# Performance work log

Measured on AMD Instinct MI355X. Metric: run time of the kernel, lower is better.

## Reference

```python
import jax, jax.numpy as jnp
import numpy as np
import math

B, L, D, H = 4, 1024, 1024, 16
HD = D // H

def setup_inputs() -> dict:
    rng = jax.random.key(0)
    ks = jax.random.split(rng, 11)
    def lin(k):
        # orthogonal-ish init not needed for numerics; normal scaled like torch default
        return jax.random.normal(k, (D, D), dtype=jnp.float32) * 0.02
    return {
        'key':   jax.random.normal(ks[0], (B, L, D), dtype=jnp.float32),
        'value': jax.random.normal(ks[1], (B, L, D), dtype=jnp.float32),
        'query': jax.random.normal(ks[2], (B, L, D), dtype=jnp.float32),
        'Wk': lin(ks[3]), 'bk': jnp.zeros((D,), jnp.float32),
        'Wq': lin(ks[4]), 'bq': jnp.zeros((D,), jnp.float32),
        'Wv': lin(ks[5]), 'bv': jnp.zeros((D,), jnp.float32),
        'Wp': lin(ks[6]), 'bp': jnp.zeros((D,), jnp.float32),
    }

def reference(key, value, query, Wk, bk, Wq, bq, Wv, bv, Wp, bp):
    # linear projections (torch Linear: x @ W.T + b)
    k = (key   @ Wk.T + bk).reshape(B, L, H, HD).transpose(0, 2, 1, 3)  # [B,H,L,hd]
    q = (query @ Wq.T + bq).reshape(B, L, H, HD).transpose(0, 2, 1, 3)
    v = (value @ Wv.T + bv).reshape(B, L, H, HD).transpose(0, 2, 1, 3)
    att = jnp.einsum('bhqd,bhkd->bhqk', q, k) * (1.0 / math.sqrt(HD))  # [B,H,L,L]
    causal = jnp.tril(jnp.ones((L, L), dtype=bool))
    att = jnp.where(causal[None, None], att, -jnp.inf)
    att = jax.nn.softmax(att, axis=-1)
    y = jnp.einsum('bhqk,bhkd->bhqd', att, v)  # [B,H,L,hd]
    y = y.transpose(0, 2, 1, 3).reshape(B, L, D)
    return y @ Wp.T + bp
```

## Files before the change

kernel.cpp:

```cpp
#include <hip/hip_runtime.h>

typedef unsigned short u16;
typedef __attribute__((ext_vector_type(8))) short bf16x8;
typedef __attribute__((ext_vector_type(4))) float f32x4;
typedef __attribute__((ext_vector_type(4))) unsigned short u16x4;

#define MFMA16 __builtin_amdgcn_mfma_f32_16x16x32_bf16

__device__ inline u16 f2bf(float f) {
    union { float f; unsigned u; } v; v.f = f;
    unsigned r = v.u + 0x7fffu + ((v.u >> 16) & 1u);
    return (u16)(r >> 16);
}

__device__ inline void gld16(const u16* g, u16* l) {
    __builtin_amdgcn_global_load_lds(
        (const __attribute__((address_space(1))) unsigned int*)g,
        (__attribute__((address_space(3))) unsigned int*)l, 16, 0, 0);
}

struct CvtArgs { const float* src[7]; u16* dst[7]; };

__global__ __launch_bounds__(256) void cvt_kernel(CvtArgs a) {
    const int z = blockIdx.z;
    const int n = (z < 3) ? 4194304 : 1048576;
    const size_t i = ((size_t)blockIdx.x * 256 + threadIdx.x) * 8;
    if (i >= (size_t)n) return;
    const float* s = a.src[z];
    float4 v0 = *(const float4*)(s + i);
    float4 v1 = *(const float4*)(s + i + 4);
    union { u16 h[8]; bf16x8 v; } o;
    o.h[0] = f2bf(v0.x); o.h[1] = f2bf(v0.y); o.h[2] = f2bf(v0.z); o.h[3] = f2bf(v0.w);
    o.h[4] = f2bf(v1.x); o.h[5] = f2bf(v1.y); o.h[6] = f2bf(v1.z); o.h[7] = f2bf(v1.w);
    *(bf16x8*)(a.dst[z] + i) = o.v;
}

struct GemmArgs { const u16* A; const u16* W; const float* bias; void* out; int epi; };
struct Gemm3Args { GemmArgs g[3]; };

__global__ __launch_bounds__(256, 2) void gemm_bt(Gemm3Args ga) {
    __shared__ u16 lA[128 * 32];
    __shared__ u16 lB[128 * 32];
    const GemmArgs g = ga.g[blockIdx.z];
    const int t = threadIdx.x, wave = t >> 6, lane = t & 63;
    const int quad = lane >> 4, l16 = lane & 15;
    const int rowsA = blockIdx.y * 128, rowsB = blockIdx.x * 128;
    const int wm = (wave >> 1) * 64, wn = (wave & 1) * 64;
    const u16* A = g.A; const u16* W = g.W;

    f32x4 acc[4][4] = {};

    for (int kb = 0; kb < 1024; kb += 32) {
#pragma unroll
        for (int i = 0; i < 2; i++) {
            int u = (i * 4 + wave) * 64 + lane;
            int row = u >> 2, cu = (u & 3) ^ (row & 3);
            gld16(A + (size_t)(rowsA + row) * 1024 + kb + cu * 8, lA + u * 8);
        }
#pragma unroll
        for (int i = 0; i < 2; i++) {
            int u = (i * 4 + wave) * 64 + lane;
            int row = u >> 2, cu = (u & 3) ^ (row & 3);
            gld16(W + (size_t)(rowsB + row) * 1024 + kb + cu * 8, lB + u * 8);
        }
        __syncthreads();

        bf16x8 af[4], bfr[4];
#pragma unroll
        for (int mi = 0; mi < 4; mi++) {
            int row = wm + mi * 16 + l16;
            af[mi] = *(const bf16x8*)(lA + row * 32 + ((quad ^ (row & 3)) * 8));
        }
#pragma unroll
        for (int ni = 0; ni < 4; ni++) {
            int row = wn + ni * 16 + l16;
            bfr[ni] = *(const bf16x8*)(lB + row * 32 + ((quad ^ (row & 3)) * 8));
        }
#pragma unroll
        for (int mi = 0; mi < 4; mi++)
#pragma unroll
            for (int ni = 0; ni < 4; ni++)
                acc[mi][ni] = MFMA16(af[mi], bfr[ni], acc[mi][ni], 0, 0, 0);
        __syncthreads();
    }

    const int epi = g.epi;
#pragma unroll
    for (int ni = 0; ni < 4; ni++) {
        const int ncol = rowsB + wn + ni * 16 + l16;
        const float bv = g.bias[ncol];
        const int h = ncol >> 6, hd = ncol & 63;
#pragma unroll
        for (int mi = 0; mi < 4; mi++) {
            const int mrow0 = rowsA + wm + mi * 16 + quad * 4;
            const int b = mrow0 >> 10, l0 = mrow0 & 1023;
            if (epi == 0) {
#pragma unroll
                for (int r = 0; r < 4; r++)
                    ((u16*)g.out)[((size_t)(b * 16 + h) * 1024 + l0 + r) * 64 + hd] =
                        f2bf(acc[mi][ni][r] + bv);
            } else if (epi == 2) {
                u16x4 pk;
#pragma unroll
                for (int r = 0; r < 4; r++) pk[r] = f2bf(acc[mi][ni][r] + bv);
                *(u16x4*)((u16*)g.out + ((size_t)(b * 16 + h) * 64 + hd) * 1024 + l0) = pk;
            } else {
#pragma unroll
                for (int r = 0; r < 4; r++)
                    ((float*)g.out)[(size_t)(mrow0 + r) * 1024 + ncol] = acc[mi][ni][r] + bv;
            }
        }
    }
}

__global__ __launch_bounds__(256) void attn_kernel(const u16* __restrict__ qh,
                                                   const u16* __restrict__ kh,
                                                   const u16* __restrict__ vhT,
                                                   u16* __restrict__ y)
{
    __shared__ u16 sK[64 * 64];
    __shared__ u16 sVT[64 * 64];
    __shared__ u16 sP[4 * 16 * 72];

    const int t = threadIdx.x, wave = t >> 6, lane = t & 63;
    const int quad = lane >> 4, l16 = lane & 15;
    const int p = blockIdx.x, bh = blockIdx.y;
    const int qt0 = 15 - p, qt1 = p;
    const size_t base = (size_t)bh * 1024 * 64;
    const float scale = 0.125f;

    bf16x8 aq[2][2];
#pragma unroll
    for (int s = 0; s < 2; s++) {
        const int qoff = (s == 0 ? qt0 : qt1) * 64 + wave * 16;
#pragma unroll
        for (int kr = 0; kr < 2; kr++)
            aq[s][kr] = *(const bf16x8*)(qh + base + (size_t)(qoff + l16) * 64 + kr * 32 + quad * 8);
    }

    bf16x8 ones;
#pragma unroll
    for (int j = 0; j < 8; j++) ones[j] = (short)0x3F80;

    f32x4 o[2][4] = {};
    f32x4 lacc[2] = {};
    u16* pw = sP + wave * 16 * 72;

    for (int kb = 0; kb <= qt0; kb++) {
        const int krow0 = kb * 64;
#pragma unroll
        for (int i = 0; i < 2; i++) {
            int u = (i * 4 + wave) * 64 + lane;
            int row = u >> 3, cu = (u & 7) ^ (row & 7);
            gld16(kh + base + (size_t)(krow0 + row) * 64 + cu * 8, sK + u * 8);
        }
#pragma unroll
        for (int i = 0; i < 2; i++) {
            int u = (i * 4 + wave) * 64 + lane;
            int row = u >> 3, cu = (u & 7) ^ (row & 7);
            gld16(vhT + ((size_t)(bh * 64 + row)) * 1024 + krow0 + cu * 8, sVT + u * 8);
        }
        __syncthreads();

        bf16x8 bk[4][2], bv[4][2];
#pragma unroll
        for (int kc = 0; kc < 4; kc++) {
            int row = kc * 16 + l16;
#pragma unroll
            for (int kr = 0; kr < 2; kr++)
                bk[kc][kr] = *(const bf16x8*)(sK + row * 64 + (((kr * 4 + quad) ^ (row & 7)) * 8));
        }
#pragma unroll
        for (int nt = 0; nt < 4; nt++) {
            int row = nt * 16 + l16;
#pragma unroll
            for (int kr = 0; kr < 2; kr++)
                bv[nt][kr] = *(const bf16x8*)(sVT + row * 64 + (((kr * 4 + quad) ^ (row & 7)) * 8));
        }

        auto compute = [&](int s, int qtv) {
            const int qoff = qtv * 64 + wave * 16;
            f32x4 sc[4];
#pragma unroll
            for (int kc = 0; kc < 4; kc++) {
                f32x4 z = {};
                z = MFMA16(aq[s][0], bk[kc][0], z, 0, 0, 0);
                z = MFMA16(aq[s][1], bk[kc][1], z, 0, 0, 0);
                sc[kc] = z;
            }
            const bool diag = (kb == qtv);
#pragma unroll
            for (int kc = 0; kc < 4; kc++)
#pragma unroll
                for (int r = 0; r < 4; r++) {
                    float x = fminf(sc[kc][r] * scale, 30.f);
                    float pv = __expf(x);
                    if (diag) {
                        int kcol = krow0 + kc * 16 + l16;
                        int qrow = qoff + quad * 4 + r;
                        if (kcol > qrow) pv = 0.f;
                    }
                    pw[(quad * 4 + r) * 72 + kc * 16 + l16] = f2bf(pv);
                }
            bf16x8 ap0 = *(const bf16x8*)(pw + l16 * 72 + quad * 8);
            bf16x8 ap1 = *(const bf16x8*)(pw + l16 * 72 + 32 + quad * 8);
#pragma unroll
            for (int nt = 0; nt < 4; nt++) {
                o[s][nt] = MFMA16(ap0, bv[nt][0], o[s][nt], 0, 0, 0);
                o[s][nt] = MFMA16(ap1, bv[nt][1], o[s][nt], 0, 0, 0);
            }
            lacc[s] = MFMA16(ap0, ones, lacc[s], 0, 0, 0);
            lacc[s] = MFMA16(ap1, ones, lacc[s], 0, 0, 0);
        };

        compute(0, qt0);
        if (kb <= qt1) compute(1, qt1);
        __syncthreads();
    }

    const int b = bh >> 4, h = bh & 15;
#pragma unroll
    for (int s = 0; s < 2; s++) {
        const int qoff = (s == 0 ? qt0 : qt1) * 64 + wave * 16;
#pragma unroll
        for (int nt = 0; nt < 4; nt++)
#pragma unroll
            for (int r = 0; r < 4; r++) {
                int qrow = qoff + quad * 4 + r;
                int d = nt * 16 + l16;
                y[(size_t)(b * 1024 + qrow) * 1024 + h * 64 + d] =
                    f2bf(o[s][nt][r] / lacc[s][r]);
            }
    }
}

extern "C" void kernel_launch(void* const* d_in, const int* in_sizes, int n_in,
                              void* d_out, int out_size, void* d_ws, size_t ws_size,
                              hipStream_t stream)
{
    const float* key   = (const float*)d_in[0];
    const float* value = (const float*)d_in[1];
    const float* query = (const float*)d_in[2];
    const float* Wk = (const float*)d_in[3];
    const float* bk = (const float*)d_in[4];
    const float* Wq = (const float*)d_in[5];
    const float* bq = (const float*)d_in[6];
    const float* Wv = (const float*)d_in[7];
    const float* bv = (const float*)d_in[8];
    const float* Wp = (const float*)d_in[9];
    const float* bp = (const float*)d_in[10];

    char* ws = (char*)d_ws;
    u16* xq  = (u16*)(ws + (size_t)( 0 << 20));
    u16* xk  = (u16*)(ws + (size_t)( 8 << 20));
    u16* xv  = (u16*)(ws + (size_t)(16 << 20));
    u16* wqb = (u16*)(ws + (size_t)(24 << 20));
    u16* wkb = (u16*)(ws + (size_t)(26 << 20));
    u16* wvb = (u16*)(ws + (size_t)(28 << 20));
    u16* wpb = (u16*)(ws + (size_t)(30 << 20));
    u16* qh  = (u16*)(ws + (size_t)(32 << 20));
    u16* kh  = (u16*)(ws + (size_t)(40 << 20));
    u16* vhT = (u16*)(ws + (size_t)(48 << 20));
    u16* y   = xq;

    CvtArgs ca;
    ca.src[0] = query; ca.dst[0] = xq;
    ca.src[1] = key;   ca.dst[1] = xk;
    ca.src[2] = value; ca.dst[2] = xv;
    ca.src[3] = Wq;    ca.dst[3] = wqb;
    ca.src[4] = Wk;    ca.dst[4] = wkb;
    ca.src[5] = Wv;    ca.dst[5] = wvb;
    ca.src[6] = Wp;    ca.dst[6] = wpb;
    hipLaunchKernelGGL(cvt_kernel, dim3(2048, 1, 7), dim3(256), 0, stream, ca);

    Gemm3Args g3;
    g3.g[0] = GemmArgs{xq, wqb, bq, (void*)qh,  0};
    g3.g[1] = GemmArgs{xk, wkb, bk, (void*)kh,  0};
    g3.g[2] = GemmArgs{xv, wvb, bv, (void*)vhT, 2};
    hipLaunchKernelGGL(gemm_bt, dim3(8, 32, 3), dim3(256), 0, stream, g3);

    hipLaunchKernelGGL(attn_kernel, dim3(8, 64), dim3(256), 0, stream, qh, kh, vhT, y);

    Gemm3Args gp;
    gp.g[0] = GemmArgs{y, wpb, bp, d_out, 1};
    gp.g[1] = gp.g[0]; gp.g[2] = gp.g[0];
    hipLaunchKernelGGL(gemm_bt, dim3(8, 32, 1), dim3(256), 0, stream, gp);
}
```

Measured before the change: 211.9 us.

## Widen GEMM K-tile to 64, split projection GEMM, use exp2 softmax and cheaper bf16 rounding

The QKV GEMM now stages 64-wide K slices in LDS with an 8-way XOR swizzle and requests 3 blocks per CU. The output projection gets its own kernel with 128x64 tiles, doubling the grid to 512 blocks for better CU coverage. The attention softmax folds log2(e) into the scale and calls exp2f, and f2bf drops round-to-nearest-even in favour of plain round-half-up. These cut loop and barrier overhead and ALU work, at the cost of more LDS per block and slightly different rounding.

```diff
diff --git a/kernel.cpp b/kernel.cpp
--- a/kernel.cpp
+++ b/kernel.cpp
@@ -9,8 +9,7 @@
 
 __device__ inline u16 f2bf(float f) {
     union { float f; unsigned u; } v; v.f = f;
-    unsigned r = v.u + 0x7fffu + ((v.u >> 16) & 1u);
-    return (u16)(r >> 16);
+    return (u16)((v.u + 0x8000u) >> 16);
 }
 
 __device__ inline void gld16(const u16* g, u16* l) {
@@ -38,9 +37,9 @@
 struct GemmArgs { const u16* A; const u16* W; const float* bias; void* out; int epi; };
 struct Gemm3Args { GemmArgs g[3]; };
 
-__global__ __launch_bounds__(256, 2) void gemm_bt(Gemm3Args ga) {
-    __shared__ u16 lA[128 * 32];
-    __shared__ u16 lB[128 * 32];
+__global__ __launch_bounds__(256, 3) void gemm_qkv(Gemm3Args ga) {
+    __shared__ u16 lA[128 * 64];
+    __shared__ u16 lB[128 * 64];
     const GemmArgs g = ga.g[blockIdx.z];
     const int t = threadIdx.x, wave = t >> 6, lane = t & 63;
     const int quad = lane >> 4, l16 = lane & 15;
@@ -50,37 +49,43 @@
 
     f32x4 acc[4][4] = {};
 
-    for (int kb = 0; kb < 1024; kb += 32) {
-#pragma unroll
-        for (int i = 0; i < 2; i++) {
-            int u = (i * 4 + wave) * 64 + lane;
-            int row = u >> 2, cu = (u & 3) ^ (row & 3);
+    for (int kb = 0; kb < 1024; kb += 64) {
+#pragma unroll
+        for (int i = 0; i < 4; i++) {
+            int u = (i * 4 + wave) * 64 + lane;
+            int row = u >> 3, cu = (u & 7) ^ (row & 7);
             gld16(A + (size_t)(rowsA + row) * 1024 + kb + cu * 8, lA + u * 8);
         }
 #pragma unroll
-        for (int i = 0; i < 2; i++) {
-            int u = (i * 4 + wave) * 64 + lane;
-            int row = u >> 2, cu = (u & 3) ^ (row & 3);
+        for (int i = 0; i < 4; i++) {
+            int u = (i * 4 + wave) * 64 + lane;
+            int row = u >> 3, cu = (u & 7) ^ (row & 7);
             gld16(W + (size_t)(rowsB + row) * 1024 + kb + cu * 8, lB + u * 8);
         }
         __syncthreads();
 
-        bf16x8 af[4], bfr[4];
+        bf16x8 af[4][2], bfr[4][2];
 #pragma unroll
         for (int mi = 0; mi < 4; mi++) {
             int row = wm + mi * 16 + l16;
-            af[mi] = *(const bf16x8*)(lA + row * 32 + ((quad ^ (row & 3)) * 8));
+#pragma unroll
+            for (int kr = 0; kr < 2; kr++)
+                af[mi][kr] = *(const bf16x8*)(lA + row * 64 + (((kr * 4 + quad) ^ (row & 7)) * 8));
         }
 #pragma unroll
         for (int ni = 0; ni < 4; ni++) {
             int row = wn + ni * 16 + l16;
-            bfr[ni] = *(const bf16x8*)(lB + row * 32 + ((quad ^ (row & 3)) * 8));
+#pragma unroll
+            for (int kr = 0; kr < 2; kr++)
+                bfr[ni][kr] = *(const bf16x8*)(lB + row * 64 + (((kr * 4 + quad) ^ (row & 7)) * 8));
         }
 #pragma unroll
         for (int mi = 0; mi < 4; mi++)
 #pragma unroll
-            for (int ni = 0; ni < 4; ni++)
-                acc[mi][ni] = MFMA16(af[mi], bfr[ni], acc[mi][ni], 0, 0, 0);
+            for (int ni = 0; ni < 4; ni++) {
+                acc[mi][ni] = MFMA16(af[mi][0], bfr[ni][0], acc[mi][ni], 0, 0, 0);
+                acc[mi][ni] = MFMA16(af[mi][1], bfr[ni][1], acc[mi][ni], 0, 0, 0);
+            }
         __syncthreads();
     }
 
@@ -99,16 +104,80 @@
                 for (int r = 0; r < 4; r++)
                     ((u16*)g.out)[((size_t)(b * 16 + h) * 1024 + l0 + r) * 64 + hd] =
                         f2bf(acc[mi][ni][r] + bv);
-            } else if (epi == 2) {
+            } else {
                 u16x4 pk;
 #pragma unroll
                 for (int r = 0; r < 4; r++) pk[r] = f2bf(acc[mi][ni][r] + bv);
                 *(u16x4*)((u16*)g.out + ((size_t)(b * 16 + h) * 64 + hd) * 1024 + l0) = pk;
-            } else {
-#pragma unroll
-                for (int r = 0; r < 4; r++)
-                    ((float*)g.out)[(size_t)(mrow0 + r) * 1024 + ncol] = acc[mi][ni][r] + bv;
-            }
+            }
+        }
+    }
+}
+
+__global__ __launch_bounds__(256, 2) void gemm_p(const u16* __restrict__ A,
+                                                 const u16* __restrict__ W,
+                                                 const float* __restrict__ bias,
+                                                 float* __restrict__ out)
+{
+    __shared__ u16 lA[128 * 64];
+    __shared__ u16 lB[64 * 64];
+    const int t = threadIdx.x, wave = t >> 6, lane = t & 63;
+    const int quad = lane >> 4, l16 = lane & 15;
+    const int rowsA = blockIdx.y * 128, rowsB = blockIdx.x * 64;
+    const int wm = (wave >> 1) * 64, wn = (wave & 1) * 32;
+
+    f32x4 acc[4][2] = {};
+
+    for (int kb = 0; kb < 1024; kb += 64) {
+#pragma unroll
+        for (int i = 0; i < 4; i++) {
+            int u = (i * 4 + wave) * 64 + lane;
+            int row = u >> 3, cu = (u & 7) ^ (row & 7);
+            gld16(A + (size_t)(rowsA + row) * 1024 + kb + cu * 8, lA + u * 8);
+        }
+#pragma unroll
+        for (int i = 0; i < 2; i++) {
+            int u = (i * 4 + wave) * 64 + lane;
+            int row = u >> 3, cu = (u & 7) ^ (row & 7);
+            gld16(W + (size_t)(rowsB + row) * 1024 + kb + cu * 8, lB + u * 8);
+        }
+        __syncthreads();
+
+        bf16x8 af[4][2], bfr[2][2];
+#pragma unroll
+        for (int mi = 0; mi < 4; mi++) {
+            int row = wm + mi * 16 + l16;
+#pragma unroll
+            for (int kr = 0; kr < 2; kr++)
+                af[mi][kr] = *(const bf16x8*)(lA + row * 64 + (((kr * 4 + quad) ^ (row & 7)) * 8));
+        }
+#pragma unroll
+        for (int ni = 0; ni < 2; ni++) {
+            int row = wn + ni * 16 + l16;
+#pragma unroll
+            for (int kr = 0; kr < 2; kr++)
+                bfr[ni][kr] = *(const bf16x8*)(lB + row * 64 + (((kr * 4 + quad) ^ (row & 7)) * 8));
+        }
+#pragma unroll
+        for (int mi = 0; mi < 4; mi++)
+#pragma unroll
+            for (int ni = 0; ni < 2; ni++) {
+                acc[mi][ni] = MFMA16(af[mi][0], bfr[ni][0], acc[mi][ni], 0, 0, 0);
+                acc[mi][ni] = MFMA16(af[mi][1], bfr[ni][1], acc[mi][ni], 0, 0, 0);
+            }
+        __syncthreads();
+    }
+
+#pragma unroll
+    for (int ni = 0; ni < 2; ni++) {
+        const int ncol = rowsB + wn + ni * 16 + l16;
+        const float bv = bias[ncol];
+#pragma unroll
+        for (int mi = 0; mi < 4; mi++) {
+            const int mrow0 = rowsA + wm + mi * 16 + quad * 4;
+#pragma unroll
+            for (int r = 0; r < 4; r++)
+                out[(size_t)(mrow0 + r) * 1024 + ncol] = acc[mi][ni][r] + bv;
         }
     }
 }
@@ -127,7 +196,7 @@
     const int p = blockIdx.x, bh = blockIdx.y;
     const int qt0 = 15 - p, qt1 = p;
     const size_t base = (size_t)bh * 1024 * 64;
-    const float scale = 0.125f;
+    const float e2 = 0.18033688f;
 
     bf16x8 aq[2][2];
 #pragma unroll
@@ -193,8 +262,8 @@
             for (int kc = 0; kc < 4; kc++)
 #pragma unroll
                 for (int r = 0; r < 4; r++) {
-                    float x = fminf(sc[kc][r] * scale, 30.f);
-                    float pv = __expf(x);
+                    float x = fminf(sc[kc][r] * e2, 43.f);
+                    float pv = exp2f(x);
                     if (diag) {
                         int kcol = krow0 + kc * 16 + l16;
                         int qrow = qoff + quad * 4 + r;
@@ -277,12 +346,9 @@
     g3.g[0] = GemmArgs{xq, wqb, bq, (void*)qh,  0};
     g3.g[1] = GemmArgs{xk, wkb, bk, (void*)kh,  0};
     g3.g[2] = GemmArgs{xv, wvb, bv, (void*)vhT, 2};
-    hipLaunchKernelGGL(gemm_bt, dim3(8, 32, 3), dim3(256), 0, stream, g3);
+    hipLaunchKernelGGL(gemm_qkv, dim3(8, 32, 3), dim3(256), 0, stream, g3);
 
     hipLaunchKernelGGL(attn_kernel, dim3(8, 64), dim3(256), 0, stream, qh, kh, vhT, y);
 
-    Gemm3Args gp;
-    gp.g[0] = GemmArgs{y, wpb, bp, d_out, 1};
-    gp.g[1] = gp.g[0]; gp.g[2] = gp.g[0];
-    hipLaunchKernelGGL(gemm_bt, dim3(8, 32, 1), dim3(256), 0, stream, gp);
-}
+    hipLaunchKernelGGL(gemm_p, dim3(16, 32), dim3(256), 0, stream, y, wpb, bp, (float*)d_out);
+}
```

Result: faster. 203.9 us (-3.8%).
